# Optimization experiments

Hardware: AMD Instinct MI355X
Metric: run time of the kernel (lower is better)

The kernel has to match this reference:

```python
import jax, jax.numpy as jnp
import numpy as np

N, F, H, C = 2048, 32, 64, 2
NEG = 0.01  # leaky_relu slope
BN_EPS = 1e-5


def _bn(h, g, b):
    m = h.mean(axis=0)
    v = h.var(axis=0)  # biased, as torch BN uses for normalization
    return (h - m) * jax.lax.rsqrt(v + BN_EPS) * g + b


def _gin(x, src, dst, eps, Wa, ba, Wb, bb):
    # PyG GINConv: out = mlp((1+eps)*x + sum_{j->i} x_j), messages flow src->dst
    agg = jax.ops.segment_sum(x[src], dst, num_segments=N)
    h = (1.0 + eps) * x + agg
    h = jax.nn.relu(h @ Wa + ba)
    return jax.nn.relu(h @ Wb + bb)


def setup_inputs() -> dict:
    key = jax.random.key(0)
    ks = jax.random.split(key, 16)
    src_np, dst_np = np.triu_indices(N, k=1)  # torch.combinations(arange(N), r=2)
    d = {
        'x': jnp.zeros((1,), jnp.float32),
        'node_features': jax.random.uniform(ks[0], (N, F), jnp.float32),
        'eps1': jnp.zeros((), jnp.float32),
        'W1a': jax.random.normal(ks[1], (F, H), jnp.float32) * 0.1,
        'b1a': jnp.zeros((H,), jnp.float32),
        'W1b': jax.random.normal(ks[2], (H, H), jnp.float32) * 0.1,
        'b1b': jnp.zeros((H,), jnp.float32),
        'epsm': jnp.zeros((), jnp.float32),
        'Wma': jax.random.normal(ks[3], (H, H), jnp.float32) * 0.1,
        'bma': jnp.zeros((H,), jnp.float32),
        'Wmb': jax.random.normal(ks[4], (H, H), jnp.float32) * 0.1,
        'bmb': jnp.zeros((H,), jnp.float32),
        'bnm_g': jnp.ones((H,), jnp.float32),
        'bnm_b': jnp.zeros((H,), jnp.float32),
        'epsl': jnp.zeros((), jnp.float32),
        'Wla': jax.random.normal(ks[5], (H, H), jnp.float32) * 0.1,
        'bla': jnp.zeros((H,), jnp.float32),
        'Wlb': jax.random.normal(ks[6], (H, F), jnp.float32) * 0.1,
        'blb': jnp.zeros((F,), jnp.float32),
        'W5': jax.random.normal(ks[7], (F, H), jnp.float32) * 0.1,
        'b5': jnp.zeros((H,), jnp.float32),
        'bn5_g': jnp.ones((H,), jnp.float32),
        'bn5_b': jnp.zeros((H,), jnp.float32),
        'W6': jax.random.normal(ks[8], (H, C), jnp.float32) * 0.1,
        'b6': jnp.zeros((C,), jnp.float32),
        'edge_src': jnp.asarray(src_np, jnp.int32),
        'edge_dst': jnp.asarray(dst_np, jnp.int32),
    }
    return d


def reference(x, node_features, eps1, W1a, b1a, W1b, b1b,
              epsm, Wma, bma, Wmb, bmb, bnm_g, bnm_b,
              epsl, Wla, bla, Wlb, blb,
              W5, b5, bn5_g, bn5_b, W6, b6,
              edge_src, edge_dst):
    xinit = node_features
    h = node_features
    # conv1 + leaky_relu
    h = jax.nn.leaky_relu(_gin(h, edge_src, edge_dst, eps1, W1a, b1a, W1b, b1b), NEG)
    # middle conv + leaky_relu + BN
    h = _gin(h, edge_src, edge_dst, epsm, Wma, bma, Wmb, bmb)
    h = jax.nn.leaky_relu(h, NEG)
    h = _bn(h, bnm_g, bnm_b)
    # last conv (back to F channels)
    h = _gin(h, edge_src, edge_dst, epsl, Wla, bla, Wlb, blb)
    h = h + xinit
    # edge predictor: gather-mul-MLP
    x_i = h[edge_src]
    x_j = h[edge_dst]
    e = jax.nn.leaky_relu((x_i * x_j) @ W5 + b5, NEG)
    e = _bn(e, bn5_g, bn5_b)
    logits = e @ W6 + b6
    p = jax.nn.softmax(logits, axis=-1)  # [E, C]
    # scatter into symmetric dense NxNxC tensor
    probs = jnp.zeros((N, N, C), jnp.float32)
    probs = probs.at[edge_src, edge_dst].set(p)
    probs = probs.at[edge_dst, edge_src].set(p)
    return probs
```

## Files before the change

### kernel.cpp

```cpp
#include <hip/hip_runtime.h>
#include <math.h>

#define NN 2048

typedef __attribute__((ext_vector_type(8))) short short8;
typedef __attribute__((ext_vector_type(4))) float f32x4;

__device__ inline short f2bf(float x) {
  union { float f; unsigned u; } v; v.f = x;
  unsigned r = v.u + 0x7fff + ((v.u >> 16) & 1);
  return (short)(r >> 16);
}
__device__ inline float bf2f(short h) {
  union { unsigned u; float f; } t;
  t.u = ((unsigned)(unsigned short)h) << 16;
  return t.f;
}

__global__ __launch_bounds__(256) void k_init(
    const float* __restrict__ nf, const float* __restrict__ W5,
    float* __restrict__ cs1, short* __restrict__ w5hi, short* __restrict__ w5lo,
    double* __restrict__ zbase) {
  __shared__ float sm[256];
  int tid = threadIdx.x, blk = blockIdx.x;
  int gtid = blk * 256 + tid;
  int node0 = blk * 32;
  if (gtid < 10240) zbase[gtid] = 0.0;
  if (gtid < 2048) {
    int c = gtid >> 5, k = gtid & 31;
    float wv = W5[k * 64 + c];
    short hi = f2bf(wv);
    w5hi[c * 32 + k] = hi;
    w5lo[c * 32 + k] = f2bf(wv - bf2f(hi));
  }
  int f = tid & 31, g = tid >> 5;
  float acc = 0.f;
#pragma unroll
  for (int k = 0; k < 4; k++) acc += nf[(size_t)(node0 + g * 4 + k) * 32 + f];
  sm[g * 32 + f] = acc;
  __syncthreads();
  if (tid < 32) {
    float s = 0.f;
#pragma unroll
    for (int g2 = 0; g2 < 8; g2++) s += sm[g2 * 32 + tid];
    cs1[blk * 32 + tid] = s;
  }
}

template <int FIN, int FOUT, bool STATS, bool ADDX, bool AFFINE, bool CSUM>
__global__ __launch_bounds__(256) void k_mlp32(
    const float* __restrict__ X, const float* __restrict__ CS,
    const float* __restrict__ epsp,
    const float* __restrict__ Wa, const float* __restrict__ ba,
    const float* __restrict__ Wb, const float* __restrict__ bb,
    float* __restrict__ OUT, const float* __restrict__ XINIT,
    double* __restrict__ statsW, const double* __restrict__ statsRd,
    const float* __restrict__ bng, const float* __restrict__ bnb,
    float* __restrict__ csum) {
  __shared__ float xh[32 * (FIN + 1)];
  __shared__ float Ts[32 * 65];
  __shared__ float Was[FIN * 64];
  __shared__ float Wbs[64 * FOUT];
  __shared__ float spref[FIN];
  __shared__ float part[4 * FIN];
  __shared__ float bas[64];
  __shared__ float bbs[FOUT];
  __shared__ float ssum[64];
  __shared__ float ssq[64];
  __shared__ float affa[64];
  __shared__ float affb[64];
  int tid = threadIdx.x;
  int blk = blockIdx.x;
  int node0 = blk * 32;
  float ep = 1.f + epsp[0];

  if (AFFINE) {
    if (tid < 64) {
      double s1 = 0.0, s2 = 0.0;
#pragma unroll
      for (int r = 0; r < 16; r++) {
        s1 += statsRd[r * 128 + tid];
        s2 += statsRd[r * 128 + 64 + tid];
      }
      double mean = s1 * (1.0 / 2048.0);
      double var = s2 * (1.0 / 2048.0) - mean * mean;
      if (var < 0.0) var = 0.0;
      float a = (float)((double)bng[tid] / sqrt(var + 1e-5));
      affa[tid] = a;
      affb[tid] = fmaf(-(float)mean, a, bnb[tid]);
    }
    __syncthreads();
  }

  for (int idx = tid; idx < 32 * FIN / 4; idx += 256) {
    int row = idx / (FIN / 4), c4 = (idx % (FIN / 4)) * 4;
    float4 v = *(const float4*)(X + (size_t)(node0 + row) * FIN + c4);
    if (AFFINE) {
      v.x = fmaf(affa[c4 + 0], v.x, affb[c4 + 0]);
      v.y = fmaf(affa[c4 + 1], v.y, affb[c4 + 1]);
      v.z = fmaf(affa[c4 + 2], v.z, affb[c4 + 2]);
      v.w = fmaf(affa[c4 + 3], v.w, affb[c4 + 3]);
    }
    float* dst = xh + row * (FIN + 1) + c4;
    dst[0] = v.x; dst[1] = v.y; dst[2] = v.z; dst[3] = v.w;
  }
  if (tid < 4 * FIN) {
    int g = tid / FIN, f = tid % FIN;
    float s = 0.f;
    for (int c = g; c < blk; c += 4) s += CS[c * FIN + f];
    part[tid] = s;
  }
  for (int idx = tid; idx < FIN * 16; idx += 256)
    *(float4*)(Was + idx * 4) = *(const float4*)(Wa + idx * 4);
  for (int idx = tid; idx < FOUT * 16; idx += 256)
    *(float4*)(Wbs + idx * 4) = *(const float4*)(Wb + idx * 4);
  if (tid < 64) bas[tid] = ba[tid];
  if (tid < FOUT) bbs[tid] = bb[tid];
  if ((STATS || CSUM) && tid < 64) { ssum[tid] = 0.f; ssq[tid] = 0.f; }
  __syncthreads();

  if (tid < FIN) {
    float s = part[tid] + part[FIN + tid] + part[2 * FIN + tid] + part[3 * FIN + tid];
    if (AFFINE) s = fmaf(affa[tid], s, (float)(32 * blk) * affb[tid]);
    spref[tid] = s;
  }
  __syncthreads();

  {
    int w = tid >> 6, lane = tid & 63, half = lane >> 5, nl = lane & 31;
#pragma unroll
    for (int p = 0; p < FIN / 8; p++) {
      int f = w * (FIN / 4) + 2 * p + half;
      float v = xh[nl * (FIN + 1) + f];
      float s = v;
#pragma unroll
      for (int d = 1; d < 32; d <<= 1) {
        float t = __shfl_up(s, (unsigned)d, 32);
        if (nl >= d) s += t;
      }
      xh[nl * (FIN + 1) + f] = fmaf(ep, v, spref[f] + (s - v));
    }
  }
  __syncthreads();

  {
    int n = tid >> 3, c0 = (tid & 7) * 8;
    float acc[8];
#pragma unroll
    for (int k = 0; k < 8; k++) acc[k] = bas[c0 + k];
    for (int f = 0; f < FIN; f++) {
      float xv = xh[n * (FIN + 1) + f];
#pragma unroll
      for (int k = 0; k < 8; k++) acc[k] = fmaf(xv, Was[f * 64 + c0 + k], acc[k]);
    }
#pragma unroll
    for (int k = 0; k < 8; k++) Ts[n * 65 + c0 + k] = fmaxf(acc[k], 0.f);
  }
  __syncthreads();

  {
    constexpr int CC = FOUT / 8;
    int n = tid >> 3, c0 = (tid & 7) * CC;
    float acc[CC];
#pragma unroll
    for (int k = 0; k < CC; k++) acc[k] = bbs[c0 + k];
    for (int f = 0; f < 64; f++) {
      float tv = Ts[n * 65 + f];
#pragma unroll
      for (int k = 0; k < CC; k++) acc[k] = fmaf(tv, Wbs[f * FOUT + c0 + k], acc[k]);
    }
#pragma unroll
    for (int k = 0; k < CC; k++) {
      float r = fmaxf(acc[k], 0.f);
      if (STATS || CSUM) atomicAdd(&ssum[c0 + k], r);
      if (STATS) atomicAdd(&ssq[c0 + k], r * r);
      if (ADDX) r += XINIT[(size_t)(node0 + n) * FOUT + c0 + k];
      OUT[(size_t)(node0 + n) * FOUT + c0 + k] = r;
    }
  }
  if (STATS || CSUM) {
    __syncthreads();
    if (tid < FOUT) {
      if (CSUM) csum[blk * FOUT + tid] = ssum[tid];
      if (STATS) {
        int rep = blk & 15;
        atomicAdd(&statsW[rep * 128 + tid], (double)ssum[tid]);
        atomicAdd(&statsW[rep * 128 + 64 + tid], (double)ssq[tid]);
      }
    }
  }
}

__device__ inline void tile_decode(int t, int& bi, int& bj) {
  bi = (int)((257.0f - sqrtf(66049.0f - 8.0f * (float)t)) * 0.5f);
  if (bi > 127) bi = 127;
  while (bi > 0 && bi * (257 - bi) / 2 > t) bi--;
  while ((bi + 1) * (256 - bi) / 2 <= t) bi++;
  bj = bi + (t - bi * (257 - bi) / 2);
}

__device__ inline void split_pack(const float m[8], short8& ah, short8& al) {
  unsigned uh[8], ul[8];
#pragma unroll
  for (int e = 0; e < 8; e++) {
    union { float f; unsigned u; } um; um.f = m[e];
    uh[e] = um.u;
    union { unsigned u; float f; } hf; hf.u = um.u & 0xffff0000u;
    union { float f; unsigned u; } lf; lf.f = m[e] - hf.f;
    ul[e] = lf.u;
  }
  union { unsigned i[4]; short8 s; } ph, pl;
#pragma unroll
  for (int k = 0; k < 4; k++) {
    ph.i[k] = __builtin_amdgcn_perm(uh[2 * k + 1], uh[2 * k], 0x07060302u);
    pl.i[k] = __builtin_amdgcn_perm(ul[2 * k + 1], ul[2 * k], 0x07060302u);
  }
  ah = ph.s;
  al = pl.s;
}

__device__ inline f32x4 mfma3b(short8 ah, short8 al, short8 bh, short8 bl, float bias) {
  f32x4 z = (f32x4){bias, bias, bias, bias};
  z = __builtin_amdgcn_mfma_f32_16x16x32_bf16(al, bh, z, 0, 0, 0);
  z = __builtin_amdgcn_mfma_f32_16x16x32_bf16(ah, bl, z, 0, 0, 0);
  z = __builtin_amdgcn_mfma_f32_16x16x32_bf16(ah, bh, z, 0, 0, 0);
  return z;
}

__global__ __launch_bounds__(256) void k_edge1m(
    const float* __restrict__ H3, const short* __restrict__ W5Th,
    const short* __restrict__ W5Tl, const float* __restrict__ b5,
    double* __restrict__ stats5, int T, int stride) {
  __shared__ float sI[16][36];
  __shared__ float sJ[16][36];
  __shared__ float ssum[64], ssq[64];
  int tid = threadIdx.x;
  int w = tid >> 6, lane = tid & 63;
  int quad = lane >> 4, l15 = lane & 15;
  int q8 = quad * 8;
  if (tid < 64) { ssum[tid] = 0.f; ssq[tid] = 0.f; }

  short8 bh[4], bl[4];
  float b5v[4];
#pragma unroll
  for (int nt = 0; nt < 4; nt++) {
    bh[nt] = *(const short8*)(W5Th + (nt * 16 + l15) * 32 + q8);
    bl[nt] = *(const short8*)(W5Tl + (nt * 16 + l15) * 32 + q8);
    b5v[nt] = b5[nt * 16 + l15];
  }
  float accS[4] = {0.f, 0.f, 0.f, 0.f}, accQ[4] = {0.f, 0.f, 0.f, 0.f};

  for (int t = blockIdx.x; t < T; t += stride) {
    int bi, bj;
    tile_decode(t, bi, bj);
    __syncthreads();
    {
      int row = tid >> 3, c4 = (tid & 7) * 4;
      int grow = (row < 16) ? (bi * 16 + row) : (bj * 16 + row - 16);
      float4 v = *(const float4*)(H3 + (size_t)grow * 32 + c4);
      float* dst = (row < 16) ? &sI[row][c4] : &sJ[row - 16][c4];
      *(float4*)dst = v;
    }
    __syncthreads();
    const float* pJ = &sJ[l15][q8];
    float4 j0 = *(const float4*)pJ, j1 = *(const float4*)(pJ + 4);
    short8 ah[4], al[4];
#pragma unroll
    for (int mt = 0; mt < 4; mt++) {
      const float* pI = &sI[4 * w + mt][q8];
      float4 i0 = *(const float4*)pI, i1 = *(const float4*)(pI + 4);
      float m[8] = {i0.x * j0.x, i0.y * j0.y, i0.z * j0.z, i0.w * j0.w,
                    i1.x * j1.x, i1.y * j1.y, i1.z * j1.z, i1.w * j1.w};
      split_pack(m, ah[mt], al[mt]);
    }
    bool diag = (bi == bj);
#pragma unroll
    for (int mt = 0; mt < 4; mt++) {
      int iRow = bi * 16 + 4 * w + mt;
#pragma unroll
      for (int nt = 0; nt < 4; nt++) {
        f32x4 z = mfma3b(ah[mt], al[mt], bh[nt], bl[nt], b5v[nt]);
#pragma unroll
        for (int r = 0; r < 4; r++) {
          float e = fmaxf(z[r], z[r] * 0.01f);
          if (diag) {
            int jCol = bj * 16 + quad * 4 + r;
            e = (iRow < jCol) ? e : 0.f;
          }
          accS[nt] += e;
          accQ[nt] = fmaf(e, e, accQ[nt]);
        }
      }
    }
  }
#pragma unroll
  for (int nt = 0; nt < 4; nt++) {
    accS[nt] += __shfl_xor(accS[nt], 16); accS[nt] += __shfl_xor(accS[nt], 32);
    accQ[nt] += __shfl_xor(accQ[nt], 16); accQ[nt] += __shfl_xor(accQ[nt], 32);
  }
  if (quad == 0) {
#pragma unroll
    for (int nt = 0; nt < 4; nt++) {
      atomicAdd(&ssum[nt * 16 + l15], accS[nt]);
      atomicAdd(&ssq[nt * 16 + l15], accQ[nt]);
    }
  }
  __syncthreads();
  if (tid < 64) {
    int rep = blockIdx.x & 63;
    atomicAdd(&stats5[rep * 128 + tid], (double)ssum[tid]);
    atomicAdd(&stats5[rep * 128 + 64 + tid], (double)ssq[tid]);
  }
}

__global__ void k_prep5(const double* __restrict__ stats5, const float* __restrict__ g,
                        const float* __restrict__ bb, const float* __restrict__ W6,
                        const float* __restrict__ b6, float* __restrict__ prep,
                        double ecnt) {
  __shared__ float sdel[64];
  int c = threadIdx.x;
  if (c < 64) {
    double s1 = 0.0, s2 = 0.0;
    for (int r = 0; r < 64; r++) {
      s1 += stats5[r * 128 + c];
      s2 += stats5[r * 128 + 64 + c];
    }
    double mean = s1 / ecnt;
    double var = s2 / ecnt - mean * mean;
    if (var < 0.0) var = 0.0;
    float a = (float)((double)g[c] / sqrt(var + 1e-5));
    float sh = (float)((double)bb[c] - mean * (double)a);
    float dw = W6[2 * c + 1] - W6[2 * c];
    prep[c] = a * dw;
    sdel[c] = sh * dw;
  }
  __syncthreads();
  if (c == 0) {
    float t = b6[1] - b6[0];
    for (int k = 0; k < 64; k++) t += sdel[k];
    prep[64] = t;
  }
}

__global__ __launch_bounds__(256) void k_edge2m(
    const float* __restrict__ H3, const short* __restrict__ W5Th,
    const short* __restrict__ W5Tl, const float* __restrict__ b5,
    const float* __restrict__ prep, float* __restrict__ outp) {
  __shared__ float sI[16][36];
  __shared__ float sJ[16][36];
  int tid = threadIdx.x;
  int w = tid >> 6, lane = tid & 63;
  int quad = lane >> 4, l15 = lane & 15;
  int q8 = quad * 8;
  int bi, bj;
  tile_decode(blockIdx.x, bi, bj);
  {
    int row = tid >> 3, c4 = (tid & 7) * 4;
    int grow = (row < 16) ? (bi * 16 + row) : (bj * 16 + row - 16);
    float4 v = *(const float4*)(H3 + (size_t)grow * 32 + c4);
    float* dst = (row < 16) ? &sI[row][c4] : &sJ[row - 16][c4];
    *(float4*)dst = v;
  }
  short8 ah[4], al[4];
  f32x4 b5v[4], uv[4];
#pragma unroll
  for (int Mt = 0; Mt < 4; Mt++) {
    ah[Mt] = *(const short8*)(W5Th + (Mt * 16 + l15) * 32 + q8);
    al[Mt] = *(const short8*)(W5Tl + (Mt * 16 + l15) * 32 + q8);
    b5v[Mt] = *(const f32x4*)(b5 + Mt * 16 + quad * 4);
    uv[Mt] = *(const f32x4*)(prep + Mt * 16 + quad * 4);
  }
  float dbase = prep[64];
  __syncthreads();

  const float* pJ = &sJ[l15][q8];
  float4 j0 = *(const float4*)pJ, j1 = *(const float4*)(pJ + 4);
  float dkeep = 0.f;
#pragma unroll
  for (int nt = 0; nt < 4; nt++) {
    const float* pI = &sI[4 * w + nt][q8];
    float4 i0 = *(const float4*)pI, i1 = *(const float4*)(pI + 4);
    float m[8] = {i0.x * j0.x, i0.y * j0.y, i0.z * j0.z, i0.w * j0.w,
                  i1.x * j1.x, i1.y * j1.y, i1.z * j1.z, i1.w * j1.w};
    short8 bh, bl;
    split_pack(m, bh, bl);
    float d = 0.f;
#pragma unroll
    for (int Mt = 0; Mt < 4; Mt++) {
      f32x4 z = b5v[Mt];
      z = __builtin_amdgcn_mfma_f32_16x16x32_bf16(al[Mt], bh, z, 0, 0, 0);
      z = __builtin_amdgcn_mfma_f32_16x16x32_bf16(ah[Mt], bl, z, 0, 0, 0);
      z = __builtin_amdgcn_mfma_f32_16x16x32_bf16(ah[Mt], bh, z, 0, 0, 0);
#pragma unroll
      for (int r = 0; r < 4; r++) {
        float e = fmaxf(z[r], z[r] * 0.01f);
        d = fmaf(e, uv[Mt][r], d);
      }
    }
    d += __shfl_xor(d, 16);
    d += __shfl_xor(d, 32);
    if (quad == nt) dkeep = d;
  }
  int i = bi * 16 + 4 * w + quad;
  int j = bj * 16 + l15;
  if (i < j) {
    float dd = dkeep + dbase;
    float ex = __expf(dd);
    float p0 = 1.f / (1.f + ex);
    float2 p = make_float2(p0, ex * p0);
    *(float2*)(outp + ((size_t)i * NN + j) * 2) = p;
    *(float2*)(outp + ((size_t)j * NN + i) * 2) = p;
  } else if (i == j) {
    *(float2*)(outp + ((size_t)i * NN + i) * 2) = make_float2(0.f, 0.f);
  }
}

extern "C" void kernel_launch(void* const* d_in, const int* in_sizes, int n_in,
                              void* d_out, int out_size, void* d_ws, size_t ws_size,
                              hipStream_t stream) {
  const float* nf   = (const float*)d_in[1];
  const float* eps1 = (const float*)d_in[2];
  const float* W1a  = (const float*)d_in[3];
  const float* b1a  = (const float*)d_in[4];
  const float* W1b  = (const float*)d_in[5];
  const float* b1b  = (const float*)d_in[6];
  const float* epsm = (const float*)d_in[7];
  const float* Wma  = (const float*)d_in[8];
  const float* bma  = (const float*)d_in[9];
  const float* Wmb  = (const float*)d_in[10];
  const float* bmb  = (const float*)d_in[11];
  const float* bnmg = (const float*)d_in[12];
  const float* bnmb = (const float*)d_in[13];
  const float* epsl = (const float*)d_in[14];
  const float* Wla  = (const float*)d_in[15];
  const float* bla  = (const float*)d_in[16];
  const float* Wlb  = (const float*)d_in[17];
  const float* blb  = (const float*)d_in[18];
  const float* W5   = (const float*)d_in[19];
  const float* b5   = (const float*)d_in[20];
  const float* bn5g = (const float*)d_in[21];
  const float* bn5b = (const float*)d_in[22];
  const float* W6   = (const float*)d_in[23];
  const float* b6   = (const float*)d_in[24];
  double ecnt = (double)in_sizes[25];
  float* out = (float*)d_out;

  float* w = (float*)d_ws;
  float* h1   = w;
  float* h2   = w + 131072;
  float* h3   = w + 262144;
  float* cs1  = w + 327680;
  float* cs2  = w + 329728;
  float* csr  = w + 333824;
  float* prep = w + 337920;
  short* w5hi = (short*)(w + 338112);
  short* w5lo = (short*)(w + 339136);
  double* statsM = (double*)(w + 340160);
  double* stats5 = statsM + 2048;

  k_init<<<64, 256, 0, stream>>>(nf, W5, cs1, w5hi, w5lo, statsM);
  k_mlp32<32, 64, false, false, false, true><<<64, 256, 0, stream>>>(
      nf, cs1, eps1, W1a, b1a, W1b, b1b, h1, nullptr, nullptr, nullptr,
      nullptr, nullptr, cs2);
  k_mlp32<64, 64, true, false, false, true><<<64, 256, 0, stream>>>(
      h1, cs2, epsm, Wma, bma, Wmb, bmb, h2, nullptr, statsM, nullptr,
      nullptr, nullptr, csr);
  k_mlp32<64, 32, false, true, true, false><<<64, 256, 0, stream>>>(
      h2, csr, epsl, Wla, bla, Wlb, blb, h3, nf, nullptr, statsM,
      bnmg, bnmb, nullptr);

  const int T = 8256;
  const int NB = 2064;
  k_edge1m<<<NB, 256, 0, stream>>>(h3, w5hi, w5lo, b5, stats5, T, NB);
  k_prep5<<<1, 64, 0, stream>>>(stats5, bn5g, bn5b, W6, b6, prep, ecnt);
  k_edge2m<<<T, 256, 0, stream>>>(h3, w5hi, w5lo, b5, prep, out);
}
```

Baseline: 255.3 us.

## Fuse init into layer-1 MLP, fold BN prep into edge pass, trim MFMAs

Merges the init kernel with the first GIN MLP layer, recomputing each block's prefix sum over earlier node rows inside the kernel. The separate k_prep5 launch is folded into k_edge1m through a last-block-done atomic counter. The stats pass now drops one of the three split-bf16 MFMAs, so it no longer splits the activation into hi and lo parts. Both edge kernels use packed float2 math for the leaky-relu and the reductions. This trades launch overhead and matrix work for a small loss of precision in the BN5 statistics, and the prefix loop now does uneven work across blocks.

```diff
diff --git a/kernel.cpp b/kernel.cpp
--- a/kernel.cpp
+++ b/kernel.cpp
@@ -5,6 +5,7 @@
 
 typedef __attribute__((ext_vector_type(8))) short short8;
 typedef __attribute__((ext_vector_type(4))) float f32x4;
+typedef __attribute__((ext_vector_type(2))) float f32x2;
 
 __device__ inline short f2bf(float x) {
   union { float f; unsigned u; } v; v.f = x;
@@ -17,15 +18,30 @@
   return t.f;
 }
 
-__global__ __launch_bounds__(256) void k_init(
+__global__ __launch_bounds__(256) void k_l1(
     const float* __restrict__ nf, const float* __restrict__ W5,
-    float* __restrict__ cs1, short* __restrict__ w5hi, short* __restrict__ w5lo,
-    double* __restrict__ zbase) {
-  __shared__ float sm[256];
+    const float* __restrict__ epsp,
+    const float* __restrict__ Wa, const float* __restrict__ ba,
+    const float* __restrict__ Wb, const float* __restrict__ bb,
+    float* __restrict__ OUT, float* __restrict__ csum,
+    short* __restrict__ w5hi, short* __restrict__ w5lo,
+    double* __restrict__ zbase, int* __restrict__ cnt) {
+  __shared__ float xh[32 * 33];
+  __shared__ float Ts[32 * 65];
+  __shared__ float Was[32 * 64];
+  __shared__ float Wbs[64 * 64];
+  __shared__ float pr[32 * 36];
+  __shared__ float spref[32];
+  __shared__ float bas[64];
+  __shared__ float bbs[64];
+  __shared__ float ssum[64];
   int tid = threadIdx.x, blk = blockIdx.x;
   int gtid = blk * 256 + tid;
   int node0 = blk * 32;
+  float ep = 1.f + epsp[0];
+
   if (gtid < 10240) zbase[gtid] = 0.0;
+  if (gtid == 0) *cnt = 0;
   if (gtid < 2048) {
     int c = gtid >> 5, k = gtid & 31;
     float wv = W5[k * 64 + c];
@@ -33,18 +49,84 @@
     w5hi[c * 32 + k] = hi;
     w5lo[c * 32 + k] = f2bf(wv - bf2f(hi));
   }
-  int f = tid & 31, g = tid >> 5;
-  float acc = 0.f;
-#pragma unroll
-  for (int k = 0; k < 4; k++) acc += nf[(size_t)(node0 + g * 4 + k) * 32 + f];
-  sm[g * 32 + f] = acc;
+
+  {
+    int row = tid >> 3, c4 = (tid & 7) * 4;
+    float4 v = *(const float4*)(nf + (size_t)(node0 + row) * 32 + c4);
+    float* dst = xh + row * 33 + c4;
+    dst[0] = v.x; dst[1] = v.y; dst[2] = v.z; dst[3] = v.w;
+  }
+  {
+    int q = tid & 7, s = tid >> 3;
+    float a0 = 0.f, a1 = 0.f, a2 = 0.f, a3 = 0.f;
+    for (int flat = tid; flat < blk * 256; flat += 256) {
+      const float4 v = *(const float4*)(nf + (size_t)(flat >> 3) * 32 + q * 4);
+      a0 += v.x; a1 += v.y; a2 += v.z; a3 += v.w;
+    }
+    float* d = pr + s * 36 + q * 4;
+    d[0] = a0; d[1] = a1; d[2] = a2; d[3] = a3;
+  }
+  for (int idx = tid; idx < 32 * 16; idx += 256)
+    *(float4*)(Was + idx * 4) = *(const float4*)(Wa + idx * 4);
+  for (int idx = tid; idx < 64 * 16; idx += 256)
+    *(float4*)(Wbs + idx * 4) = *(const float4*)(Wb + idx * 4);
+  if (tid < 64) { bas[tid] = ba[tid]; bbs[tid] = bb[tid]; ssum[tid] = 0.f; }
   __syncthreads();
   if (tid < 32) {
     float s = 0.f;
-#pragma unroll
-    for (int g2 = 0; g2 < 8; g2++) s += sm[g2 * 32 + tid];
-    cs1[blk * 32 + tid] = s;
-  }
+    for (int r = 0; r < 32; r++) s += pr[r * 36 + tid];
+    spref[tid] = s;
+  }
+  __syncthreads();
+  {
+    int w = tid >> 6, lane = tid & 63, half = lane >> 5, nl = lane & 31;
+#pragma unroll
+    for (int p = 0; p < 4; p++) {
+      int f = w * 8 + 2 * p + half;
+      float v = xh[nl * 33 + f];
+      float s = v;
+#pragma unroll
+      for (int d = 1; d < 32; d <<= 1) {
+        float t = __shfl_up(s, (unsigned)d, 32);
+        if (nl >= d) s += t;
+      }
+      xh[nl * 33 + f] = fmaf(ep, v, spref[f] + (s - v));
+    }
+  }
+  __syncthreads();
+  {
+    int n = tid >> 3, c0 = (tid & 7) * 8;
+    float acc[8];
+#pragma unroll
+    for (int k = 0; k < 8; k++) acc[k] = bas[c0 + k];
+    for (int f = 0; f < 32; f++) {
+      float xv = xh[n * 33 + f];
+#pragma unroll
+      for (int k = 0; k < 8; k++) acc[k] = fmaf(xv, Was[f * 64 + c0 + k], acc[k]);
+    }
+#pragma unroll
+    for (int k = 0; k < 8; k++) Ts[n * 65 + c0 + k] = fmaxf(acc[k], 0.f);
+  }
+  __syncthreads();
+  {
+    int n = tid >> 3, c0 = (tid & 7) * 8;
+    float acc[8];
+#pragma unroll
+    for (int k = 0; k < 8; k++) acc[k] = bbs[c0 + k];
+    for (int f = 0; f < 64; f++) {
+      float tv = Ts[n * 65 + f];
+#pragma unroll
+      for (int k = 0; k < 8; k++) acc[k] = fmaf(tv, Wbs[f * 64 + c0 + k], acc[k]);
+    }
+#pragma unroll
+    for (int k = 0; k < 8; k++) {
+      float r = fmaxf(acc[k], 0.f);
+      atomicAdd(&ssum[c0 + k], r);
+      OUT[(size_t)(node0 + n) * 64 + c0 + k] = r;
+    }
+  }
+  __syncthreads();
+  if (tid < 64) csum[blk * 64 + tid] = ssum[tid];
 }
 
 template <int FIN, int FOUT, bool STATS, bool ADDX, bool AFFINE, bool CSUM>
@@ -219,21 +301,19 @@
   al = pl.s;
 }
 
-__device__ inline f32x4 mfma3b(short8 ah, short8 al, short8 bh, short8 bl, float bias) {
-  f32x4 z = (f32x4){bias, bias, bias, bias};
-  z = __builtin_amdgcn_mfma_f32_16x16x32_bf16(al, bh, z, 0, 0, 0);
-  z = __builtin_amdgcn_mfma_f32_16x16x32_bf16(ah, bl, z, 0, 0, 0);
-  z = __builtin_amdgcn_mfma_f32_16x16x32_bf16(ah, bh, z, 0, 0, 0);
-  return z;
-}
-
 __global__ __launch_bounds__(256) void k_edge1m(
     const float* __restrict__ H3, const short* __restrict__ W5Th,
     const short* __restrict__ W5Tl, const float* __restrict__ b5,
-    double* __restrict__ stats5, int T, int stride) {
+    double* __restrict__ stats5, int T, int stride, int* __restrict__ cnt,
+    const float* __restrict__ bn5g, const float* __restrict__ bn5b,
+    const float* __restrict__ W6, const float* __restrict__ b6,
+    float* __restrict__ prep, double ecnt) {
   __shared__ float sI[16][36];
   __shared__ float sJ[16][36];
   __shared__ float ssum[64], ssq[64];
+  __shared__ int amlast;
+  __shared__ double foldd[128];
+  __shared__ float sdel[64];
   int tid = threadIdx.x;
   int w = tid >> 6, lane = tid & 63;
   int quad = lane >> 4, l15 = lane & 15;
@@ -248,7 +328,12 @@
     bl[nt] = *(const short8*)(W5Tl + (nt * 16 + l15) * 32 + q8);
     b5v[nt] = b5[nt * 16 + l15];
   }
-  float accS[4] = {0.f, 0.f, 0.f, 0.f}, accQ[4] = {0.f, 0.f, 0.f, 0.f};
+  f32x2 aS[4], aQ[4];
+#pragma unroll
+  for (int nt = 0; nt < 4; nt++) {
+    aS[nt] = (f32x2){0.f, 0.f};
+    aQ[nt] = (f32x2){0.f, 0.f};
+  }
 
   for (int t = blockIdx.x; t < T; t += stride) {
     int bi, bj;
@@ -264,14 +349,21 @@
     __syncthreads();
     const float* pJ = &sJ[l15][q8];
     float4 j0 = *(const float4*)pJ, j1 = *(const float4*)(pJ + 4);
-    short8 ah[4], al[4];
+    short8 ah[4];
 #pragma unroll
     for (int mt = 0; mt < 4; mt++) {
       const float* pI = &sI[4 * w + mt][q8];
       float4 i0 = *(const float4*)pI, i1 = *(const float4*)(pI + 4);
-      float m[8] = {i0.x * j0.x, i0.y * j0.y, i0.z * j0.z, i0.w * j0.w,
-                    i1.x * j1.x, i1.y * j1.y, i1.z * j1.z, i1.w * j1.w};
-      split_pack(m, ah[mt], al[mt]);
+      union { float f[8]; unsigned u[8]; } p;
+      p.f[0] = i0.x * j0.x; p.f[1] = i0.y * j0.y;
+      p.f[2] = i0.z * j0.z; p.f[3] = i0.w * j0.w;
+      p.f[4] = i1.x * j1.x; p.f[5] = i1.y * j1.y;
+      p.f[6] = i1.z * j1.z; p.f[7] = i1.w * j1.w;
+      union { unsigned i[4]; short8 s; } pk;
+#pragma unroll
+      for (int k = 0; k < 4; k++)
+        pk.i[k] = __builtin_amdgcn_perm(p.u[2 * k + 1], p.u[2 * k], 0x07060302u);
+      ah[mt] = pk.s;
     }
     bool diag = (bi == bj);
 #pragma unroll
@@ -279,22 +371,37 @@
       int iRow = bi * 16 + 4 * w + mt;
 #pragma unroll
       for (int nt = 0; nt < 4; nt++) {
-        f32x4 z = mfma3b(ah[mt], al[mt], bh[nt], bl[nt], b5v[nt]);
-#pragma unroll
-        for (int r = 0; r < 4; r++) {
-          float e = fmaxf(z[r], z[r] * 0.01f);
-          if (diag) {
+        float bb = b5v[nt];
+        f32x4 z = (f32x4){bb, bb, bb, bb};
+        z = __builtin_amdgcn_mfma_f32_16x16x32_bf16(ah[mt], bl[nt], z, 0, 0, 0);
+        z = __builtin_amdgcn_mfma_f32_16x16x32_bf16(ah[mt], bh[nt], z, 0, 0, 0);
+        if (diag) {
+          float er[4];
+#pragma unroll
+          for (int r = 0; r < 4; r++) {
+            float e = fmaxf(z[r], z[r] * 0.01f);
             int jCol = bj * 16 + quad * 4 + r;
-            e = (iRow < jCol) ? e : 0.f;
+            er[r] = (iRow < jCol) ? e : 0.f;
           }
-          accS[nt] += e;
-          accQ[nt] = fmaf(e, e, accQ[nt]);
+          aS[nt] += (f32x2){er[0] + er[2], er[1] + er[3]};
+          aQ[nt] += (f32x2){er[0] * er[0] + er[2] * er[2],
+                            er[1] * er[1] + er[3] * er[3]};
+        } else {
+          f32x2 za = (f32x2){z[0], z[1]}, zb = (f32x2){z[2], z[3]};
+          f32x2 ea = __builtin_elementwise_max(za, za * 0.01f);
+          f32x2 eb = __builtin_elementwise_max(zb, zb * 0.01f);
+          aS[nt] += ea + eb;
+          aQ[nt] += ea * ea;
+          aQ[nt] += eb * eb;
         }
       }
     }
   }
+  float accS[4], accQ[4];
 #pragma unroll
   for (int nt = 0; nt < 4; nt++) {
+    accS[nt] = aS[nt][0] + aS[nt][1];
+    accQ[nt] = aQ[nt][0] + aQ[nt][1];
     accS[nt] += __shfl_xor(accS[nt], 16); accS[nt] += __shfl_xor(accS[nt], 32);
     accQ[nt] += __shfl_xor(accQ[nt], 16); accQ[nt] += __shfl_xor(accQ[nt], 32);
   }
@@ -311,34 +418,35 @@
     atomicAdd(&stats5[rep * 128 + tid], (double)ssum[tid]);
     atomicAdd(&stats5[rep * 128 + 64 + tid], (double)ssq[tid]);
   }
-}
-
-__global__ void k_prep5(const double* __restrict__ stats5, const float* __restrict__ g,
-                        const float* __restrict__ bb, const float* __restrict__ W6,
-                        const float* __restrict__ b6, float* __restrict__ prep,
-                        double ecnt) {
-  __shared__ float sdel[64];
-  int c = threadIdx.x;
-  if (c < 64) {
-    double s1 = 0.0, s2 = 0.0;
-    for (int r = 0; r < 64; r++) {
-      s1 += stats5[r * 128 + c];
-      s2 += stats5[r * 128 + 64 + c];
-    }
-    double mean = s1 / ecnt;
-    double var = s2 / ecnt - mean * mean;
-    if (var < 0.0) var = 0.0;
-    float a = (float)((double)g[c] / sqrt(var + 1e-5));
-    float sh = (float)((double)bb[c] - mean * (double)a);
-    float dw = W6[2 * c + 1] - W6[2 * c];
-    prep[c] = a * dw;
-    sdel[c] = sh * dw;
-  }
-  __syncthreads();
-  if (c == 0) {
-    float t = b6[1] - b6[0];
-    for (int k = 0; k < 64; k++) t += sdel[k];
-    prep[64] = t;
+  __threadfence();
+  if (tid == 0) amlast = (atomicAdd(cnt, 1) == (int)gridDim.x - 1) ? 1 : 0;
+  __syncthreads();
+  if (amlast) {
+    __threadfence();
+    if (tid < 128) {
+      int c = tid & 63, kind = tid >> 6;
+      const volatile double* sp = stats5 + kind * 64 + c;
+      double s = 0.0;
+      for (int r = 0; r < 64; r++) s += sp[r * 128];
+      foldd[tid] = s;
+    }
+    __syncthreads();
+    if (tid < 64) {
+      double mean = foldd[tid] / ecnt;
+      double var = foldd[64 + tid] / ecnt - mean * mean;
+      if (var < 0.0) var = 0.0;
+      float a = (float)((double)bn5g[tid] / sqrt(var + 1e-5));
+      float sh = (float)((double)bn5b[tid] - mean * (double)a);
+      float dwc = W6[2 * tid + 1] - W6[2 * tid];
+      prep[tid] = a * dwc;
+      sdel[tid] = sh * dwc;
+    }
+    __syncthreads();
+    if (tid == 0) {
+      float t = b6[1] - b6[0];
+      for (int k = 0; k < 64; k++) t += sdel[k];
+      prep[64] = t;
+    }
   }
 }
 
@@ -384,19 +492,22 @@
                   i1.x * j1.x, i1.y * j1.y, i1.z * j1.z, i1.w * j1.w};
     short8 bh, bl;
     split_pack(m, bh, bl);
-    float d = 0.f;
+    f32x2 d2 = (f32x2){0.f, 0.f};
 #pragma unroll
     for (int Mt = 0; Mt < 4; Mt++) {
       f32x4 z = b5v[Mt];
       z = __builtin_amdgcn_mfma_f32_16x16x32_bf16(al[Mt], bh, z, 0, 0, 0);
       z = __builtin_amdgcn_mfma_f32_16x16x32_bf16(ah[Mt], bl, z, 0, 0, 0);
       z = __builtin_amdgcn_mfma_f32_16x16x32_bf16(ah[Mt], bh, z, 0, 0, 0);
-#pragma unroll
-      for (int r = 0; r < 4; r++) {
-        float e = fmaxf(z[r], z[r] * 0.01f);
-        d = fmaf(e, uv[Mt][r], d);
-      }
-    }
+      f32x2 za = (f32x2){z[0], z[1]}, zb = (f32x2){z[2], z[3]};
+      f32x2 ea = __builtin_elementwise_max(za, za * 0.01f);
+      f32x2 eb = __builtin_elementwise_max(zb, zb * 0.01f);
+      f32x2 ua = (f32x2){uv[Mt][0], uv[Mt][1]};
+      f32x2 ub = (f32x2){uv[Mt][2], uv[Mt][3]};
+      d2 += ea * ua;
+      d2 += eb * ub;
+    }
+    float d = d2[0] + d2[1];
     d += __shfl_xor(d, 16);
     d += __shfl_xor(d, 32);
     if (quad == nt) dkeep = d;
@@ -449,19 +560,17 @@
   float* h1   = w;
   float* h2   = w + 131072;
   float* h3   = w + 262144;
-  float* cs1  = w + 327680;
-  float* cs2  = w + 329728;
-  float* csr  = w + 333824;
-  float* prep = w + 337920;
-  short* w5hi = (short*)(w + 338112);
-  short* w5lo = (short*)(w + 339136);
-  double* statsM = (double*)(w + 340160);
+  float* cs2  = w + 327680;
+  float* csr  = w + 331776;
+  float* prep = w + 335872;
+  int*   cnt  = (int*)(w + 336000);
+  short* w5hi = (short*)(w + 336064);
+  short* w5lo = (short*)(w + 337088);
+  double* statsM = (double*)(w + 338112);
   double* stats5 = statsM + 2048;
 
-  k_init<<<64, 256, 0, stream>>>(nf, W5, cs1, w5hi, w5lo, statsM);
-  k_mlp32<32, 64, false, false, false, true><<<64, 256, 0, stream>>>(
-      nf, cs1, eps1, W1a, b1a, W1b, b1b, h1, nullptr, nullptr, nullptr,
-      nullptr, nullptr, cs2);
+  k_l1<<<64, 256, 0, stream>>>(nf, W5, eps1, W1a, b1a, W1b, b1b, h1, cs2,
+                               w5hi, w5lo, statsM, cnt);
   k_mlp32<64, 64, true, false, false, true><<<64, 256, 0, stream>>>(
       h1, cs2, epsm, Wma, bma, Wmb, bmb, h2, nullptr, statsM, nullptr,
       nullptr, nullptr, csr);
@@ -471,7 +580,7 @@
 
   const int T = 8256;
   const int NB = 2064;
-  k_edge1m<<<NB, 256, 0, stream>>>(h3, w5hi, w5lo, b5, stats5, T, NB);
-  k_prep5<<<1, 64, 0, stream>>>(stats5, bn5g, bn5b, W6, b6, prep, ecnt);
+  k_edge1m<<<NB, 256, 0, stream>>>(h3, w5hi, w5lo, b5, stats5, T, NB, cnt,
+                                   bn5g, bn5b, W6, b6, prep, ecnt);
   k_edge2m<<<T, 256, 0, stream>>>(h3, w5hi, w5lo, b5, prep, out);
 }
```

New measurement: 369.1 us. +44.6%, slower.
